# Optimization experiments

Hardware: AMD Instinct MI355X
Metric: run time of the kernel (lower is better)

## Reference

```python
import jax, jax.numpy as jnp
import numpy as np

N, E, F_IN, D, H, G, T = 30000, 480000, 128, 32, 4, 128, 10
HD = H * D
NEG_SLOPE = 0.2


def _lin(key, fan_out, fan_in, scale=0.05):
    k1, k2 = jax.random.split(key)
    return (jax.random.normal(k1, (fan_out, fan_in), jnp.float32) * scale,
            jax.random.normal(k2, (fan_out,), jnp.float32) * scale)


def setup_inputs() -> dict:
    key = jax.random.key(0)
    ks = jax.random.split(key, 24)
    x = jax.random.normal(ks[0], (N, F_IN), jnp.float32)
    edge_index = jax.random.randint(ks[1], (2, E), 0, N, jnp.int64)
    batch = jnp.sort(jax.random.randint(ks[2], (N,), 0, G, jnp.int64))
    inp = {"x": x, "edge_index": edge_index, "batch": batch}
    # conv 0 (in=F_IN) and conv 1 (in=D); each followed by Linear(HD -> D)
    for i, fin in enumerate([F_IN, D]):
        base = 3 + i * 8
        Wl, bl = _lin(ks[base + 0], HD, fin)
        Wr, br = _lin(ks[base + 1], HD, fin)
        att = jax.random.normal(ks[base + 2], (H, D), jnp.float32) * 0.05
        bias = jnp.zeros((HD,), jnp.float32)
        lw, lb = _lin(ks[base + 3], D, HD)
        inp.update({f"Wl{i}": Wl, f"bl{i}": bl, f"Wr{i}": Wr, f"br{i}": br,
                    f"att{i}": att, f"cb{i}": bias, f"lw{i}": lw, f"lb{i}": lb})
    inp["fc1_W"], inp["fc1_b"] = _lin(ks[20], D, D)
    inp["fc2_W"], inp["fc2_b"] = _lin(ks[21], T, D)
    return inp


def _gatv2_conv(x, src, dst, Wl, bl, Wr, br, att, bias):
    # PyG GATv2Conv, concat=True, add_self_loops already applied to src/dst,
    # aggr='mean', eval mode (no dropout).
    n = x.shape[0]
    xl = (x @ Wl.T + bl).reshape(n, H, D)
    xr = (x @ Wr.T + br).reshape(n, H, D)
    e = jax.nn.leaky_relu(xl[src] + xr[dst], NEG_SLOPE)          # [E', H, D]
    alpha = jnp.einsum('ehd,hd->eh', e, att)                      # [E', H]
    amax = jax.ops.segment_max(alpha, dst, num_segments=n)        # [n, H]
    ex = jnp.exp(alpha - amax[dst])
    denom = jax.ops.segment_sum(ex, dst, num_segments=n)
    a = ex / denom[dst]                                           # softmax per target
    msg = xl[src] * a[:, :, None]                                 # [E', H, D]
    s = jax.ops.segment_sum(msg, dst, num_segments=n)
    cnt = jax.ops.segment_sum(jnp.ones((src.shape[0],), jnp.float32), dst, num_segments=n)
    out = s / cnt[:, None, None]                                  # mean aggregation
    return out.reshape(n, HD) + bias


def reference(x, edge_index, batch,
              Wl0, bl0, Wr0, br0, att0, cb0, lw0, lb0,
              Wl1, bl1, Wr1, br1, att1, cb1, lw1, lb1,
              fc1_W, fc1_b, fc2_W, fc2_b):
    loop = jnp.arange(N, dtype=edge_index.dtype)
    src = jnp.concatenate([edge_index[0], loop])  # add self loops
    dst = jnp.concatenate([edge_index[1], loop])
    convs = [(Wl0, bl0, Wr0, br0, att0, cb0, lw0, lb0),
             (Wl1, bl1, Wr1, br1, att1, cb1, lw1, lb1)]
    h = x
    for (Wl, bl, Wr, br, att, cb, lw, lb) in convs:
        h = _gatv2_conv(h, src, dst, Wl, bl, Wr, br, att, cb)
        h = h @ lw.T + lb  # heads>1: Linear(H*D -> D)
    g = jax.ops.segment_max(h, batch, num_segments=G)  # global max pool
    g = jax.nn.relu(g @ fc1_W.T + fc1_b)
    return g @ fc2_W.T + fc2_b
```

## Files before the change

### kernel.cpp

```cpp
#include <hip/hip_runtime.h>
#include <hip/hip_bf16.h>
#include <hip/hip_fp16.h>

#define NEG_SLOPE 0.2f
#define GGRP 128
#define TOUT 10

typedef _Float16 half8 __attribute__((ext_vector_type(8)));
typedef float floatx4 __attribute__((ext_vector_type(4)));

__global__ void init_kernel(int* __restrict__ deg, float* __restrict__ gpool,
                            int* __restrict__ csr_pad, int n, int gsize) {
    int i = blockIdx.x * blockDim.x + threadIdx.x;
    if (i < n) deg[i] = 0;
    if (i < gsize) gpool[i] = -__builtin_inff();
    if (i < 64) csr_pad[i] = 0;
}

__global__ void cvt_kernel(const float* __restrict__ X, _Float16* __restrict__ Xh,
                           const float* __restrict__ Wl, _Float16* __restrict__ Wlh,
                           const float* __restrict__ Wr, _Float16* __restrict__ Wrh,
                           int nx8, int nw8) {
    int i = blockIdx.x * blockDim.x + threadIdx.x;
    const float* s; _Float16* d; int j;
    if (i < nx8) { s = X; d = Xh; j = i; }
    else if (i < nx8 + nw8) { s = Wl; d = Wlh; j = i - nx8; }
    else if (i < nx8 + 2 * nw8) { s = Wr; d = Wrh; j = i - nx8 - nw8; }
    else return;
    float4 a = *(const float4*)(s + j * 8);
    float4 b = *(const float4*)(s + j * 8 + 4);
    union { _Float16 h[8]; uint4 u; } pk;
    pk.h[0] = (_Float16)a.x; pk.h[1] = (_Float16)a.y;
    pk.h[2] = (_Float16)a.z; pk.h[3] = (_Float16)a.w;
    pk.h[4] = (_Float16)b.x; pk.h[5] = (_Float16)b.y;
    pk.h[6] = (_Float16)b.z; pk.h[7] = (_Float16)b.w;
    *(uint4*)(d + j * 8) = pk.u;
}

__global__ void degree_kernel(const int* __restrict__ dst, int* __restrict__ deg, int E) {
    int i = blockIdx.x * blockDim.x + threadIdx.x;
    int base = i * 4;
    if (base + 3 < E) {
        int4 d = *(const int4*)(dst + base);
        atomicAdd(&deg[d.x], 1); atomicAdd(&deg[d.y], 1);
        atomicAdd(&deg[d.z], 1); atomicAdd(&deg[d.w], 1);
    } else {
        for (int k = base; k < E; ++k) atomicAdd(&deg[dst[k]], 1);
    }
}

__global__ __launch_bounds__(256)
void scanA_kernel(const int* __restrict__ deg, int* __restrict__ rowptr,
                  int* __restrict__ bsum, int n) {
    __shared__ int wsum[4];
    int tid = threadIdx.x, lane = tid & 63, wid = tid >> 6;
    int idx = blockIdx.x * 256 + tid;
    int v = (idx < n) ? deg[idx] : 0;
    int x = v;
    #pragma unroll
    for (int off = 1; off < 64; off <<= 1) {
        int t = __shfl_up(x, off, 64);
        if (lane >= off) x += t;
    }
    if (lane == 63) wsum[wid] = x;
    __syncthreads();
    if (tid == 0) {
        int s = 0;
        #pragma unroll
        for (int i = 0; i < 4; ++i) { int t = wsum[i]; wsum[i] = s; s += t; }
        bsum[blockIdx.x] = s;
    }
    __syncthreads();
    int excl = x - v + wsum[wid];
    if (idx < n) rowptr[idx] = excl;
}

__global__ __launch_bounds__(256)
void scanC_kernel(int* __restrict__ rowptr, int* __restrict__ cursor,
                  const int* __restrict__ bsum, int n, int nb) {
    __shared__ int soff_sh;
    int tid = threadIdx.x;
    int bx = blockIdx.x;
    if (tid < 64) {
        int lane = tid;
        int v = 0;
        if (lane < nb && lane < bx) v = bsum[lane];
        if (lane + 64 < nb && lane + 64 < bx) v += bsum[lane + 64];
        #pragma unroll
        for (int off = 32; off >= 1; off >>= 1) v += __shfl_xor(v, off, 64);
        if (lane == 0) soff_sh = v;
        if (bx == 0) {
            int t = 0;
            if (lane < nb) t = bsum[lane];
            if (lane + 64 < nb) t += bsum[lane + 64];
            #pragma unroll
            for (int off = 32; off >= 1; off >>= 1) t += __shfl_xor(t, off, 64);
            if (lane == 0) rowptr[n] = t;
        }
    }
    __syncthreads();
    int idx = bx * 256 + tid;
    if (idx < n) {
        int r = rowptr[idx] + soff_sh;
        rowptr[idx] = r;
        cursor[idx] = r;
    }
}

__global__ void scatter_kernel(const int* __restrict__ src, const int* __restrict__ dst,
                               int* __restrict__ cursor, int* __restrict__ csr, int E) {
    int i = blockIdx.x * blockDim.x + threadIdx.x;
    int base = i * 4;
    if (base + 3 < E) {
        int4 s = *(const int4*)(src + base);
        int4 d = *(const int4*)(dst + base);
        csr[atomicAdd(&cursor[d.x], 1)] = s.x << 8;
        csr[atomicAdd(&cursor[d.y], 1)] = s.y << 8;
        csr[atomicAdd(&cursor[d.z], 1)] = s.z << 8;
        csr[atomicAdd(&cursor[d.w], 1)] = s.w << 8;
    } else {
        for (int k = base; k < E; ++k)
            csr[atomicAdd(&cursor[dst[k]], 1)] = src[k] << 8;
    }
}

__global__ __launch_bounds__(256)
void gemm_mfma_kernel(const _Float16* __restrict__ Xh,
                      const _Float16* __restrict__ Wlh, const float* __restrict__ bl,
                      const _Float16* __restrict__ Wrh, const float* __restrict__ br,
                      _Float16* __restrict__ xlh, float* __restrict__ xr, int n) {
    int tid = threadIdx.x;
    int wave = tid >> 6, lane = tid & 63;
    int r0 = blockIdx.x * 64 + wave * 16;
    if (r0 >= n) return;
    int l15 = lane & 15;
    int lkg = lane >> 4;
    int arow = r0 + l15; if (arow > n - 1) arow = n - 1;

    const char* xb  = (const char*)Xh;
    const char* wlb = (const char*)Wlh;
    const char* wrb = (const char*)Wrh;

    half8 a[4];
    #pragma unroll
    for (int kc = 0; kc < 4; ++kc)
        a[kc] = *(const half8*)(xb + (size_t)arow * 256 + kc * 64 + lkg * 16);

    floatx4 accL[8], accR[8];
    #pragma unroll
    for (int t = 0; t < 8; ++t) {
        accL[t] = (floatx4){0.f, 0.f, 0.f, 0.f};
        accR[t] = (floatx4){0.f, 0.f, 0.f, 0.f};
    }

    #pragma unroll
    for (int t = 0; t < 8; ++t) {
        int wrow = t * 16 + l15;
        int wk = lkg * 16;
        #pragma unroll
        for (int kc = 0; kc < 4; ++kc) {
            half8 bL = *(const half8*)(wlb + (size_t)wrow * 256 + kc * 64 + wk);
            half8 bR = *(const half8*)(wrb + (size_t)wrow * 256 + kc * 64 + wk);
            accL[t] = __builtin_amdgcn_mfma_f32_16x16x32_f16(a[kc], bL, accL[t], 0, 0, 0);
            accR[t] = __builtin_amdgcn_mfma_f32_16x16x32_f16(a[kc], bR, accR[t], 0, 0, 0);
        }
    }

    #pragma unroll
    for (int j = 0; j < 4; ++j) {
        int row = r0 + lkg * 4 + j;
        if (row < n) {
            #pragma unroll
            for (int t = 0; t < 8; ++t) {
                int col = t * 16 + l15;
                float vL = accL[t][j] + bl[col];
                float vR = accR[t][j] + br[col];
                xlh[(size_t)row * 128 + col] = (_Float16)vL;
                xr[(size_t)row * 128 + col] = vR;
            }
        }
    }
}

template <int FIN>
__global__ __launch_bounds__(256, 2)
void gemm_tile_kernel(const float* __restrict__ X,
                      const float* __restrict__ Wl, const float* __restrict__ bl,
                      const float* __restrict__ Wr, const float* __restrict__ br,
                      _Float16* __restrict__ xlh, float* __restrict__ xr,
                      int n, int nRowBlk) {
    constexpr int BK = 32, BM = 128, LDA = BM + 4;
    constexpr int NCHUNK = FIN / BK;
    __shared__ float Xs[BK][LDA];
    __shared__ float Ws[BK][LDA];
    int tid = threadIdx.x;
    int rowBlk = blockIdx.x;
    int colBlk = 0;
    if (rowBlk >= nRowBlk) { rowBlk -= nRowBlk; colBlk = 1; }
    const float* __restrict__ Wb = colBlk ? Wr : Wl;
    const float* __restrict__ bb = colBlk ? br : bl;
    int row0 = rowBlk * BM;

    int sr  = tid >> 3;
    int skq = (tid & 7) * 4;

    float4 xpre[4], wpre[4];

    auto load_pre = [&](int c) {
        int k0 = c * BK;
        #pragma unroll
        for (int i = 0; i < 4; ++i) {
            int r = sr + i * 32;
            int gr = row0 + r;
            float4 v = {0.f, 0.f, 0.f, 0.f};
            if (gr < n) v = *(const float4*)&X[(size_t)gr * FIN + k0 + skq];
            xpre[i] = v;
            wpre[i] = *(const float4*)&Wb[(size_t)r * FIN + k0 + skq];
        }
    };
    auto store_pre = [&]() {
        #pragma unroll
        for (int i = 0; i < 4; ++i) {
            int r = sr + i * 32;
            Xs[skq + 0][r] = xpre[i].x; Xs[skq + 1][r] = xpre[i].y;
            Xs[skq + 2][r] = xpre[i].z; Xs[skq + 3][r] = xpre[i].w;
            Ws[skq + 0][r] = wpre[i].x; Ws[skq + 1][r] = wpre[i].y;
            Ws[skq + 2][r] = wpre[i].z; Ws[skq + 3][r] = wpre[i].w;
        }
    };

    load_pre(0);
    store_pre();
    __syncthreads();

    int tx = tid & 15;
    int ty = tid >> 4;
    float acc[8][8];
    #pragma unroll
    for (int i = 0; i < 8; ++i)
        #pragma unroll
        for (int j = 0; j < 8; ++j) acc[i][j] = 0.f;

    #pragma unroll
    for (int c = 0; c < NCHUNK; ++c) {
        if (c + 1 < NCHUNK) load_pre(c + 1);
        #pragma unroll 8
        for (int k = 0; k < BK; ++k) {
            float4 a0 = *(const float4*)&Xs[k][ty * 8];
            float4 a1 = *(const float4*)&Xs[k][ty * 8 + 4];
            float4 b0 = *(const float4*)&Ws[k][tx * 8];
            float4 b1 = *(const float4*)&Ws[k][tx * 8 + 4];
            float av[8] = {a0.x, a0.y, a0.z, a0.w, a1.x, a1.y, a1.z, a1.w};
            float bv[8] = {b0.x, b0.y, b0.z, b0.w, b1.x, b1.y, b1.z, b1.w};
            #pragma unroll
            for (int i = 0; i < 8; ++i)
                #pragma unroll
                for (int j = 0; j < 8; ++j)
                    acc[i][j] = fmaf(av[i], bv[j], acc[i][j]);
        }
        if (c + 1 < NCHUNK) {
            __syncthreads();
            store_pre();
            __syncthreads();
        }
    }

    float bias[8];
    #pragma unroll
    for (int j = 0; j < 8; ++j) bias[j] = bb[tx * 8 + j];
    #pragma unroll
    for (int i = 0; i < 8; ++i) {
        int gr = row0 + ty * 8 + i;
        if (gr < n) {
            float v[8];
            #pragma unroll
            for (int j = 0; j < 8; ++j) v[j] = acc[i][j] + bias[j];
            if (colBlk == 0) {
                union { _Float16 h[8]; uint4 u; } pk;
                #pragma unroll
                for (int j = 0; j < 8; ++j) pk.h[j] = (_Float16)v[j];
                *(uint4*)&xlh[(size_t)gr * 128 + tx * 8] = pk.u;
            } else {
                float4 o0 = {v[0], v[1], v[2], v[3]};
                float4 o1 = {v[4], v[5], v[6], v[7]};
                *(float4*)&xr[(size_t)gr * 128 + tx * 8]     = o0;
                *(float4*)&xr[(size_t)gr * 128 + tx * 8 + 4] = o1;
            }
        }
    }
}

__global__ __launch_bounds__(256)
void gat_fused_kernel(const _Float16* __restrict__ xlh,
                      const float* __restrict__ xr,
                      const float* __restrict__ att, const float* __restrict__ cb,
                      const float* __restrict__ lw, const float* __restrict__ lb,
                      const int* __restrict__ rowptr, const int* __restrict__ csrb,
                      float* __restrict__ out , int n) {
    __shared__ float lws[32][132];
    __shared__ float oslot[4][128];
    int tid = threadIdx.x;
    #pragma unroll
    for (int i = 0; i < 16; ++i) {
        int idx = tid + i * 256;
        lws[idx >> 7][idx & 127] = lw[idx];
    }
    __syncthreads();

    int wid = tid >> 6, lane = tid & 63;
    int nd = blockIdx.x * 4 + wid;
    if (nd >= n) return;
    int q4  = lane >> 4;
    int l16 = lane & 15;
    int fb  = l16 * 32;
    int fbh = l16 * 16;

    const char* __restrict__ xlhb = (const char*)xlh;
    const char* __restrict__ xrb  = (const char*)xr;

    const float4 xrA = *(const float4*)(xrb + ((size_t)nd << 9) + fb);
    const float4 xrB = *(const float4*)(xrb + ((size_t)nd << 9) + fb + 16);
    const float4 atA = *(const float4*)((const char*)att + fb);
    const float4 atB = *(const float4*)((const char*)att + fb + 16);

    float4 xlsA, xlsB;
    {
        uint4 hs = *(const uint4*)(xlhb + ((size_t)nd << 8) + fbh);
        float2 s01 = __half22float2(*(const __half2*)&hs.x);
        float2 s23 = __half22float2(*(const __half2*)&hs.y);
        float2 s45 = __half22float2(*(const __half2*)&hs.z);
        float2 s67 = __half22float2(*(const __half2*)&hs.w);
        xlsA = (float4){s01.x, s01.y, s23.x, s23.y};
        xlsB = (float4){s45.x, s45.y, s67.x, s67.y};
    }

    int start = rowptr[nd], end = rowptr[nd + 1];
    float cnt = (float)(end - start + 1);

    float den;
    float accA[4], accB[4];

    {
        float e0 = xlsA.x + xrA.x; e0 = fmaxf(e0, NEG_SLOPE * e0);
        float e1 = xlsA.y + xrA.y; e1 = fmaxf(e1, NEG_SLOPE * e1);
        float e2 = xlsA.z + xrA.z; e2 = fmaxf(e2, NEG_SLOPE * e2);
        float e3 = xlsA.w + xrA.w; e3 = fmaxf(e3, NEG_SLOPE * e3);
        float e4 = xlsB.x + xrB.x; e4 = fmaxf(e4, NEG_SLOPE * e4);
        float e5 = xlsB.y + xrB.y; e5 = fmaxf(e5, NEG_SLOPE * e5);
        float e6 = xlsB.z + xrB.z; e6 = fmaxf(e6, NEG_SLOPE * e6);
        float e7 = xlsB.w + xrB.w; e7 = fmaxf(e7, NEG_SLOPE * e7);
        float q = e0 * atA.x + e1 * atA.y + e2 * atA.z + e3 * atA.w
                + e4 * atB.x + e5 * atB.y + e6 * atB.z + e7 * atB.w;
        q += __shfl_xor(q, 1); q += __shfl_xor(q, 2);
        float a = __expf(q);
        if (q4 == 0) {
            den = a;
            accA[0] = a * xlsA.x; accA[1] = a * xlsA.y;
            accA[2] = a * xlsA.z; accA[3] = a * xlsA.w;
            accB[0] = a * xlsB.x; accB[1] = a * xlsB.y;
            accB[2] = a * xlsB.z; accB[3] = a * xlsB.w;
        } else {
            den = 0.f;
            accA[0] = accA[1] = accA[2] = accA[3] = 0.f;
            accB[0] = accB[1] = accB[2] = accB[3] = 0.f;
        }
    }

    auto consume = [&](uint4 hx, bool guard) {
        float2 f01 = __half22float2(*(const __half2*)&hx.x);
        float2 f23 = __half22float2(*(const __half2*)&hx.y);
        float2 f45 = __half22float2(*(const __half2*)&hx.z);
        float2 f67 = __half22float2(*(const __half2*)&hx.w);
        float e0 = f01.x + xrA.x; e0 = fmaxf(e0, NEG_SLOPE * e0);
        float e1 = f01.y + xrA.y; e1 = fmaxf(e1, NEG_SLOPE * e1);
        float e2 = f23.x + xrA.z; e2 = fmaxf(e2, NEG_SLOPE * e2);
        float e3 = f23.y + xrA.w; e3 = fmaxf(e3, NEG_SLOPE * e3);
        float e4 = f45.x + xrB.x; e4 = fmaxf(e4, NEG_SLOPE * e4);
        float e5 = f45.y + xrB.y; e5 = fmaxf(e5, NEG_SLOPE * e5);
        float e6 = f67.x + xrB.z; e6 = fmaxf(e6, NEG_SLOPE * e6);
        float e7 = f67.y + xrB.w; e7 = fmaxf(e7, NEG_SLOPE * e7);
        float q = e0 * atA.x + e1 * atA.y + e2 * atA.z + e3 * atA.w
                + e4 * atB.x + e5 * atB.y + e6 * atB.z + e7 * atB.w;
        q += __shfl_xor(q, 1); q += __shfl_xor(q, 2);
        float a = __expf(q);
        if (!guard) a = 0.f;
        den += a;
        accA[0] = fmaf(a, f01.x, accA[0]); accA[1] = fmaf(a, f01.y, accA[1]);
        accA[2] = fmaf(a, f23.x, accA[2]); accA[3] = fmaf(a, f23.y, accA[3]);
        accB[0] = fmaf(a, f45.x, accB[0]); accB[1] = fmaf(a, f45.y, accB[1]);
        accB[2] = fmaf(a, f67.x, accB[2]); accB[3] = fmaf(a, f67.y, accB[3]);
    };

    int i = start + q4;
    int oA = csrb[i], oB = csrb[i + 4], oC = csrb[i + 8], oD = csrb[i + 12];
    uint4 pA = *(const uint4*)(xlhb + oA + fbh);
    uint4 pB = *(const uint4*)(xlhb + oB + fbh);
    uint4 pC = *(const uint4*)(xlhb + oC + fbh);
    uint4 pD = *(const uint4*)(xlhb + oD + fbh);
    oA = csrb[i + 16]; oB = csrb[i + 20]; oC = csrb[i + 24]; oD = csrb[i + 28];
    for (; i < end; i += 16) {
        uint4 c0 = pA;
        pA = *(const uint4*)(xlhb + oA + fbh); oA = csrb[i + 32];
        consume(c0, true);
        uint4 c1 = pB;
        pB = *(const uint4*)(xlhb + oB + fbh); oB = csrb[i + 36];
        consume(c1, (i + 4) < end);
        uint4 c2 = pC;
        pC = *(const uint4*)(xlhb + oC + fbh); oC = csrb[i + 40];
        consume(c2, (i + 8) < end);
        uint4 c3 = pD;
        pD = *(const uint4*)(xlhb + oD + fbh); oD = csrb[i + 44];
        consume(c3, (i + 12) < end);
    }

    #pragma unroll
    for (int t = 0; t < 4; ++t) {
        accA[t] += __shfl_xor(accA[t], 16); accA[t] += __shfl_xor(accA[t], 32);
        accB[t] += __shfl_xor(accB[t], 16); accB[t] += __shfl_xor(accB[t], 32);
    }
    den += __shfl_xor(den, 16); den += __shfl_xor(den, 32);

    float inv = 1.0f / (den * cnt);
    if (q4 == 0) {
        const float4 cbA = *(const float4*)((const char*)cb + fb);
        const float4 cbB = *(const float4*)((const char*)cb + fb + 16);
        float4 oA4, oB4;
        oA4.x = fmaf(accA[0], inv, cbA.x); oA4.y = fmaf(accA[1], inv, cbA.y);
        oA4.z = fmaf(accA[2], inv, cbA.z); oA4.w = fmaf(accA[3], inv, cbA.w);
        oB4.x = fmaf(accB[0], inv, cbB.x); oB4.y = fmaf(accB[1], inv, cbB.y);
        oB4.z = fmaf(accB[2], inv, cbB.z); oB4.w = fmaf(accB[3], inv, cbB.w);
        *(float4*)((char*)&oslot[wid][0] + fb)      = oA4;
        *(float4*)((char*)&oslot[wid][0] + fb + 16) = oB4;
    }
    asm volatile("s_waitcnt lgkmcnt(0)" ::: "memory");

    int half = lane >> 5;
    int l32 = lane & 31;
    float y = 0.f;
    int kbase = half * 64;
    #pragma unroll
    for (int k = 0; k < 64; k += 4) {
        float4 lv = *(const float4*)&lws[l32][kbase + k];
        float4 ov = *(const float4*)&oslot[wid][kbase + k];
        y = fmaf(lv.x, ov.x, y);
        y = fmaf(lv.y, ov.y, y);
        y = fmaf(lv.z, ov.z, y);
        y = fmaf(lv.w, ov.w, y);
    }
    y += __shfl_xor(y, 32);
    if (half == 0) out[(size_t)nd * 32 + l32] = y + lb[l32];
}

__device__ __forceinline__ void atomicMaxFloat(float* addr, float val) {
    if (val >= 0.f) atomicMax((int*)addr, __float_as_int(val));
    else atomicMin((unsigned int*)addr, (unsigned int)__float_as_int(val));
}

__global__ void pool_kernel(const float* __restrict__ H, const int* __restrict__ batch,
                            float* __restrict__ g, int n) {
    int tid = threadIdx.x;
    int dim = tid & 31;
    int sub = tid >> 5;
    int nodeStart = blockIdx.x * 128 + sub * 16;
    float m = -__builtin_inff();
    int cur = -1;
    for (int j = 0; j < 16; ++j) {
        int nd = nodeStart + j;
        if (nd >= n) break;
        int b = batch[nd];
        if (b != cur) {
            if (cur >= 0) atomicMaxFloat(&g[cur * 32 + dim], m);
            cur = b; m = -__builtin_inff();
        }
        m = fmaxf(m, H[nd * 32 + dim]);
    }
    if (cur >= 0) atomicMaxFloat(&g[cur * 32 + dim], m);
}

__global__ __launch_bounds__(256)
void fc_kernel(const float* __restrict__ g,
               const float* __restrict__ fc1W, const float* __restrict__ fc1b,
               const float* __restrict__ fc2W, const float* __restrict__ fc2b,
               float* __restrict__ out) {
    __shared__ float g1[GGRP * 32];
    int tid = threadIdx.x;
    for (int idx = tid; idx < GGRP * 32; idx += 256) {
        int r = idx >> 5, c = idx & 31;
        float acc = fc1b[c];
        #pragma unroll
        for (int k = 0; k < 32; ++k) acc = fmaf(g[r * 32 + k], fc1W[c * 32 + k], acc);
        g1[idx] = acc > 0.f ? acc : 0.f;
    }
    __syncthreads();
    for (int idx = tid; idx < GGRP * TOUT; idx += 256) {
        int r = idx / TOUT, c = idx - r * TOUT;
        float acc = fc2b[c];
        #pragma unroll
        for (int k = 0; k < 32; ++k) acc = fmaf(g1[r * 32 + k], fc2W[c * 32 + k], acc);
        out[idx] = acc;
    }
}

extern "C" void kernel_launch(void* const* d_in, const int* in_sizes, int n_in,
                              void* d_out, int out_size, void* d_ws, size_t ws_size,
                              hipStream_t stream) {
    const float* x     = (const float*)d_in[0];
    const int*   ei    = (const int*)d_in[1];
    const int*   batch = (const int*)d_in[2];
    const float* Wl0 = (const float*)d_in[3];
    const float* bl0 = (const float*)d_in[4];
    const float* Wr0 = (const float*)d_in[5];
    const float* br0 = (const float*)d_in[6];
    const float* at0 = (const float*)d_in[7];
    const float* cb0 = (const float*)d_in[8];
    const float* lw0 = (const float*)d_in[9];
    const float* lb0 = (const float*)d_in[10];
    const float* Wl1 = (const float*)d_in[11];
    const float* bl1 = (const float*)d_in[12];
    const float* Wr1 = (const float*)d_in[13];
    const float* br1 = (const float*)d_in[14];
    const float* at1 = (const float*)d_in[15];
    const float* cb1 = (const float*)d_in[16];
    const float* lw1 = (const float*)d_in[17];
    const float* lb1 = (const float*)d_in[18];
    const float* fc1W = (const float*)d_in[19];
    const float* fc1b = (const float*)d_in[20];
    const float* fc2W = (const float*)d_in[21];
    const float* fc2b = (const float*)d_in[22];

    const int n = in_sizes[0] / 128;
    const int E = in_sizes[1] / 2;
    const int* src = ei;
    const int* dst = ei + E;
    const int nblkScan = (n + 255) / 256;
    const int nRowBlk = (n + 127) / 128;
    const int E4 = (E + 3) / 4;
    const int nx8 = n * 16;
    const int nw8 = 128 * 128 / 8;

    size_t off = 0;
    auto alloc = [&](size_t bytes) {
        void* p = (char*)d_ws + off;
        off += (bytes + 255) & ~(size_t)255;
        return p;
    };
    _Float16* xh  = (_Float16*)alloc((size_t)n * 128 * 2);
    _Float16* wlh = (_Float16*)alloc(128 * 128 * 2);
    _Float16* wrh = (_Float16*)alloc(128 * 128 * 2);
    _Float16* xlh = (_Float16*)alloc((size_t)n * 128 * 2);
    float* xr    = (float*)alloc((size_t)n * 128 * 4);
    float* hbuf  = (float*)alloc((size_t)n * 32 * 4);
    int* deg     = (int*)alloc((size_t)n * 4);
    int* rowptr  = (int*)alloc((size_t)(n + 1) * 4);
    int* cursor  = (int*)alloc((size_t)n * 4);
    int* csr     = (int*)alloc((size_t)(E + 64) * 4);
    int* bsum    = (int*)alloc(128 * 4);
    float* gpool = (float*)alloc((size_t)GGRP * 32 * 4);

    init_kernel<<<(n + 255) / 256, 256, 0, stream>>>(deg, gpool, csr + E, n, GGRP * 32);
    cvt_kernel<<<(nx8 + 2 * nw8 + 255) / 256, 256, 0, stream>>>(x, xh, Wl0, wlh,
                                                                Wr0, wrh, nx8, nw8);
    degree_kernel<<<(E4 + 255) / 256, 256, 0, stream>>>(dst, deg, E);
    scanA_kernel<<<nblkScan, 256, 0, stream>>>(deg, rowptr, bsum, n);
    scanC_kernel<<<nblkScan, 256, 0, stream>>>(rowptr, cursor, bsum, n, nblkScan);
    scatter_kernel<<<(E4 + 255) / 256, 256, 0, stream>>>(src, dst, cursor, csr, E);

    gemm_mfma_kernel<<<(n + 63) / 64, 256, 0, stream>>>(xh, wlh, bl0, wrh, br0,
                                                        xlh, xr, n);
    gat_fused_kernel<<<(n + 3) / 4, 256, 0, stream>>>(xlh, xr, at0, cb0, lw0, lb0,
                                                      rowptr, csr, hbuf, n);
    gemm_tile_kernel<32><<<2 * nRowBlk, 256, 0, stream>>>(hbuf, Wl1, bl1, Wr1, br1,
                                                          xlh, xr, n, nRowBlk);
    gat_fused_kernel<<<(n + 3) / 4, 256, 0, stream>>>(xlh, xr, at1, cb1, lw1, lb1,
                                                      rowptr, csr, hbuf, n);

    pool_kernel<<<(n + 127) / 128, 256, 0, stream>>>(hbuf, batch, gpool, n);
    fc_kernel<<<1, 256, 0, stream>>>(gpool, fc1W, fc1b, fc2W, fc2b, (float*)d_out);
}
```

Baseline: 305.0 us.

## Use fp16 MFMA for second-layer projection and simplify gather prefetch loop

```diff
diff --git a/kernel.cpp b/kernel.cpp
--- a/kernel.cpp
+++ b/kernel.cpp
@@ -18,14 +18,18 @@
 }
 
 __global__ void cvt_kernel(const float* __restrict__ X, _Float16* __restrict__ Xh,
-                           const float* __restrict__ Wl, _Float16* __restrict__ Wlh,
-                           const float* __restrict__ Wr, _Float16* __restrict__ Wrh,
-                           int nx8, int nw8) {
+                           const float* __restrict__ Wl0, _Float16* __restrict__ Wl0h,
+                           const float* __restrict__ Wr0, _Float16* __restrict__ Wr0h,
+                           const float* __restrict__ Wl1, _Float16* __restrict__ Wl1h,
+                           const float* __restrict__ Wr1, _Float16* __restrict__ Wr1h,
+                           int nx8, int nw8, int nw1) {
     int i = blockIdx.x * blockDim.x + threadIdx.x;
     const float* s; _Float16* d; int j;
     if (i < nx8) { s = X; d = Xh; j = i; }
-    else if (i < nx8 + nw8) { s = Wl; d = Wlh; j = i - nx8; }
-    else if (i < nx8 + 2 * nw8) { s = Wr; d = Wrh; j = i - nx8 - nw8; }
+    else if (i < nx8 + nw8) { s = Wl0; d = Wl0h; j = i - nx8; }
+    else if (i < nx8 + 2 * nw8) { s = Wr0; d = Wr0h; j = i - nx8 - nw8; }
+    else if (i < nx8 + 2 * nw8 + nw1) { s = Wl1; d = Wl1h; j = i - nx8 - 2 * nw8; }
+    else if (i < nx8 + 2 * nw8 + 2 * nw1) { s = Wr1; d = Wr1h; j = i - nx8 - 2 * nw8 - nw1; }
     else return;
     float4 a = *(const float4*)(s + j * 8);
     float4 b = *(const float4*)(s + j * 8 + 4);
@@ -182,109 +186,43 @@
     }
 }
 
-template <int FIN>
-__global__ __launch_bounds__(256, 2)
-void gemm_tile_kernel(const float* __restrict__ X,
-                      const float* __restrict__ Wl, const float* __restrict__ bl,
-                      const float* __restrict__ Wr, const float* __restrict__ br,
-                      _Float16* __restrict__ xlh, float* __restrict__ xr,
-                      int n, int nRowBlk) {
-    constexpr int BK = 32, BM = 128, LDA = BM + 4;
-    constexpr int NCHUNK = FIN / BK;
-    __shared__ float Xs[BK][LDA];
-    __shared__ float Ws[BK][LDA];
+__global__ __launch_bounds__(256)
+void gemm_mfma32_kernel(const _Float16* __restrict__ Hh,
+                        const _Float16* __restrict__ Wlh, const float* __restrict__ bl,
+                        const _Float16* __restrict__ Wrh, const float* __restrict__ br,
+                        _Float16* __restrict__ xlh, float* __restrict__ xr, int n) {
     int tid = threadIdx.x;
-    int rowBlk = blockIdx.x;
-    int colBlk = 0;
-    if (rowBlk >= nRowBlk) { rowBlk -= nRowBlk; colBlk = 1; }
-    const float* __restrict__ Wb = colBlk ? Wr : Wl;
-    const float* __restrict__ bb = colBlk ? br : bl;
-    int row0 = rowBlk * BM;
-
-    int sr  = tid >> 3;
-    int skq = (tid & 7) * 4;
-
-    float4 xpre[4], wpre[4];
-
-    auto load_pre = [&](int c) {
-        int k0 = c * BK;
-        #pragma unroll
-        for (int i = 0; i < 4; ++i) {
-            int r = sr + i * 32;
-            int gr = row0 + r;
-            float4 v = {0.f, 0.f, 0.f, 0.f};
-            if (gr < n) v = *(const float4*)&X[(size_t)gr * FIN + k0 + skq];
-            xpre[i] = v;
-            wpre[i] = *(const float4*)&Wb[(size_t)r * FIN + k0 + skq];
-        }
-    };
-    auto store_pre = [&]() {
-        #pragma unroll
-        for (int i = 0; i < 4; ++i) {
-            int r = sr + i * 32;
-            Xs[skq + 0][r] = xpre[i].x; Xs[skq + 1][r] = xpre[i].y;
-            Xs[skq + 2][r] = xpre[i].z; Xs[skq + 3][r] = xpre[i].w;
-            Ws[skq + 0][r] = wpre[i].x; Ws[skq + 1][r] = wpre[i].y;
-            Ws[skq + 2][r] = wpre[i].z; Ws[skq + 3][r] = wpre[i].w;
-        }
-    };
-
-    load_pre(0);
-    store_pre();
-    __syncthreads();
-
-    int tx = tid & 15;
-    int ty = tid >> 4;
-    float acc[8][8];
-    #pragma unroll
-    for (int i = 0; i < 8; ++i)
-        #pragma unroll
-        for (int j = 0; j < 8; ++j) acc[i][j] = 0.f;
-
-    #pragma unroll
-    for (int c = 0; c < NCHUNK; ++c) {
-        if (c + 1 < NCHUNK) load_pre(c + 1);
-        #pragma unroll 8
-        for (int k = 0; k < BK; ++k) {
-            float4 a0 = *(const float4*)&Xs[k][ty * 8];
-            float4 a1 = *(const float4*)&Xs[k][ty * 8 + 4];
-            float4 b0 = *(const float4*)&Ws[k][tx * 8];
-            float4 b1 = *(const float4*)&Ws[k][tx * 8 + 4];
-            float av[8] = {a0.x, a0.y, a0.z, a0.w, a1.x, a1.y, a1.z, a1.w};
-            float bv[8] = {b0.x, b0.y, b0.z, b0.w, b1.x, b1.y, b1.z, b1.w};
+    int wave = tid >> 6, lane = tid & 63;
+    int r0 = blockIdx.x * 64 + wave * 16;
+    if (r0 >= n) return;
+    int l15 = lane & 15;
+    int lkg = lane >> 4;
+    int arow = r0 + l15; if (arow > n - 1) arow = n - 1;
+
+    half8 a = *(const half8*)(Hh + (size_t)arow * 32 + lkg * 8);
+
+    floatx4 accL[8], accR[8];
+    #pragma unroll
+    for (int t = 0; t < 8; ++t) {
+        int wrow = t * 16 + l15;
+        half8 bL = *(const half8*)(Wlh + (size_t)wrow * 32 + lkg * 8);
+        half8 bR = *(const half8*)(Wrh + (size_t)wrow * 32 + lkg * 8);
+        floatx4 z = (floatx4){0.f, 0.f, 0.f, 0.f};
+        accL[t] = __builtin_amdgcn_mfma_f32_16x16x32_f16(a, bL, z, 0, 0, 0);
+        accR[t] = __builtin_amdgcn_mfma_f32_16x16x32_f16(a, bR, z, 0, 0, 0);
+    }
+
+    #pragma unroll
+    for (int j = 0; j < 4; ++j) {
+        int row = r0 + lkg * 4 + j;
+        if (row < n) {
             #pragma unroll
-            for (int i = 0; i < 8; ++i)
-                #pragma unroll
-                for (int j = 0; j < 8; ++j)
-                    acc[i][j] = fmaf(av[i], bv[j], acc[i][j]);
-        }
-        if (c + 1 < NCHUNK) {
-            __syncthreads();
-            store_pre();
-            __syncthreads();
-        }
-    }
-
-    float bias[8];
-    #pragma unroll
-    for (int j = 0; j < 8; ++j) bias[j] = bb[tx * 8 + j];
-    #pragma unroll
-    for (int i = 0; i < 8; ++i) {
-        int gr = row0 + ty * 8 + i;
-        if (gr < n) {
-            float v[8];
-            #pragma unroll
-            for (int j = 0; j < 8; ++j) v[j] = acc[i][j] + bias[j];
-            if (colBlk == 0) {
-                union { _Float16 h[8]; uint4 u; } pk;
-                #pragma unroll
-                for (int j = 0; j < 8; ++j) pk.h[j] = (_Float16)v[j];
-                *(uint4*)&xlh[(size_t)gr * 128 + tx * 8] = pk.u;
-            } else {
-                float4 o0 = {v[0], v[1], v[2], v[3]};
-                float4 o1 = {v[4], v[5], v[6], v[7]};
-                *(float4*)&xr[(size_t)gr * 128 + tx * 8]     = o0;
-                *(float4*)&xr[(size_t)gr * 128 + tx * 8 + 4] = o1;
+            for (int t = 0; t < 8; ++t) {
+                int col = t * 16 + l15;
+                float vL = accL[t][j] + bl[col];
+                float vR = accR[t][j] + br[col];
+                xlh[(size_t)row * 128 + col] = (_Float16)vL;
+                xr[(size_t)row * 128 + col] = vR;
             }
         }
     }
@@ -296,7 +234,8 @@
                       const float* __restrict__ att, const float* __restrict__ cb,
                       const float* __restrict__ lw, const float* __restrict__ lb,
                       const int* __restrict__ rowptr, const int* __restrict__ csrb,
-                      float* __restrict__ out , int n) {
+                      float* __restrict__ out ,
+                      _Float16* __restrict__ outh , int n) {
     __shared__ float lws[32][132];
     __shared__ float oslot[4][128];
     int tid = threadIdx.x;
@@ -366,7 +305,15 @@
         }
     }
 
-    auto consume = [&](uint4 hx, bool guard) {
+    int i = start + q4;
+    int offC = csrb[i + 8];
+    uint4 preA = *(const uint4*)(xlhb + csrb[i] + fbh);
+    uint4 preB = *(const uint4*)(xlhb + csrb[i + 4] + fbh);
+    for (; i < end; i += 4) {
+        uint4 hx = preA;
+        preA = preB;
+        preB = *(const uint4*)(xlhb + offC + fbh);
+        offC = csrb[i + 12];
         float2 f01 = __half22float2(*(const __half2*)&hx.x);
         float2 f23 = __half22float2(*(const __half2*)&hx.y);
         float2 f45 = __half22float2(*(const __half2*)&hx.z);
@@ -383,34 +330,11 @@
                 + e4 * atB.x + e5 * atB.y + e6 * atB.z + e7 * atB.w;
         q += __shfl_xor(q, 1); q += __shfl_xor(q, 2);
         float a = __expf(q);
-        if (!guard) a = 0.f;
         den += a;
         accA[0] = fmaf(a, f01.x, accA[0]); accA[1] = fmaf(a, f01.y, accA[1]);
         accA[2] = fmaf(a, f23.x, accA[2]); accA[3] = fmaf(a, f23.y, accA[3]);
         accB[0] = fmaf(a, f45.x, accB[0]); accB[1] = fmaf(a, f45.y, accB[1]);
         accB[2] = fmaf(a, f67.x, accB[2]); accB[3] = fmaf(a, f67.y, accB[3]);
-    };
-
-    int i = start + q4;
-    int oA = csrb[i], oB = csrb[i + 4], oC = csrb[i + 8], oD = csrb[i + 12];
-    uint4 pA = *(const uint4*)(xlhb + oA + fbh);
-    uint4 pB = *(const uint4*)(xlhb + oB + fbh);
-    uint4 pC = *(const uint4*)(xlhb + oC + fbh);
-    uint4 pD = *(const uint4*)(xlhb + oD + fbh);
-    oA = csrb[i + 16]; oB = csrb[i + 20]; oC = csrb[i + 24]; oD = csrb[i + 28];
-    for (; i < end; i += 16) {
-        uint4 c0 = pA;
-        pA = *(const uint4*)(xlhb + oA + fbh); oA = csrb[i + 32];
-        consume(c0, true);
-        uint4 c1 = pB;
-        pB = *(const uint4*)(xlhb + oB + fbh); oB = csrb[i + 36];
-        consume(c1, (i + 4) < end);
-        uint4 c2 = pC;
-        pC = *(const uint4*)(xlhb + oC + fbh); oC = csrb[i + 40];
-        consume(c2, (i + 8) < end);
-        uint4 c3 = pD;
-        pD = *(const uint4*)(xlhb + oD + fbh); oD = csrb[i + 44];
-        consume(c3, (i + 12) < end);
     }
 
     #pragma unroll
@@ -448,7 +372,11 @@
         y = fmaf(lv.w, ov.w, y);
     }
     y += __shfl_xor(y, 32);
-    if (half == 0) out[(size_t)nd * 32 + l32] = y + lb[l32];
+    if (half == 0) {
+        float yy = y + lb[l32];
+        out[(size_t)nd * 32 + l32] = yy;
+        outh[(size_t)nd * 32 + l32] = (_Float16)yy;
+    }
 }
 
 __device__ __forceinline__ void atomicMaxFloat(float* addr, float val) {
@@ -533,10 +461,10 @@
     const int* src = ei;
     const int* dst = ei + E;
     const int nblkScan = (n + 255) / 256;
-    const int nRowBlk = (n + 127) / 128;
     const int E4 = (E + 3) / 4;
     const int nx8 = n * 16;
     const int nw8 = 128 * 128 / 8;
+    const int nw1 = 128 * 32 / 8;
 
     size_t off = 0;
     auto alloc = [&](size_t bytes) {
@@ -544,12 +472,15 @@
         off += (bytes + 255) & ~(size_t)255;
         return p;
     };
-    _Float16* xh  = (_Float16*)alloc((size_t)n * 128 * 2);
-    _Float16* wlh = (_Float16*)alloc(128 * 128 * 2);
-    _Float16* wrh = (_Float16*)alloc(128 * 128 * 2);
-    _Float16* xlh = (_Float16*)alloc((size_t)n * 128 * 2);
+    _Float16* xh   = (_Float16*)alloc((size_t)n * 128 * 2);
+    _Float16* wl0h = (_Float16*)alloc(128 * 128 * 2);
+    _Float16* wr0h = (_Float16*)alloc(128 * 128 * 2);
+    _Float16* wl1h = (_Float16*)alloc(128 * 32 * 2);
+    _Float16* wr1h = (_Float16*)alloc(128 * 32 * 2);
+    _Float16* xlh  = (_Float16*)alloc((size_t)n * 128 * 2);
     float* xr    = (float*)alloc((size_t)n * 128 * 4);
     float* hbuf  = (float*)alloc((size_t)n * 32 * 4);
+    _Float16* hbufh = (_Float16*)alloc((size_t)n * 32 * 2);
     int* deg     = (int*)alloc((size_t)n * 4);
     int* rowptr  = (int*)alloc((size_t)(n + 1) * 4);
     int* cursor  = (int*)alloc((size_t)n * 4);
@@ -558,21 +489,21 @@
     float* gpool = (float*)alloc((size_t)GGRP * 32 * 4);
 
     init_kernel<<<(n + 255) / 256, 256, 0, stream>>>(deg, gpool, csr + E, n, GGRP * 32);
-    cvt_kernel<<<(nx8 + 2 * nw8 + 255) / 256, 256, 0, stream>>>(x, xh, Wl0, wlh,
-                                                                Wr0, wrh, nx8, nw8);
+    cvt_kernel<<<(nx8 + 2 * nw8 + 2 * nw1 + 255) / 256, 256, 0, stream>>>(
+        x, xh, Wl0, wl0h, Wr0, wr0h, Wl1, wl1h, Wr1, wr1h, nx8, nw8, nw1);
     degree_kernel<<<(E4 + 255) / 256, 256, 0, stream>>>(dst, deg, E);
     scanA_kernel<<<nblkScan, 256, 0, stream>>>(deg, rowptr, bsum, n);
     scanC_kernel<<<nblkScan, 256, 0, stream>>>(rowptr, cursor, bsum, n, nblkScan);
     scatter_kernel<<<(E4 + 255) / 256, 256, 0, stream>>>(src, dst, cursor, csr, E);
 
-    gemm_mfma_kernel<<<(n + 63) / 64, 256, 0, stream>>>(xh, wlh, bl0, wrh, br0,
+    gemm_mfma_kernel<<<(n + 63) / 64, 256, 0, stream>>>(xh, wl0h, bl0, wr0h, br0,
                                                         xlh, xr, n);
     gat_fused_kernel<<<(n + 3) / 4, 256, 0, stream>>>(xlh, xr, at0, cb0, lw0, lb0,
-                                                      rowptr, csr, hbuf, n);
-    gemm_tile_kernel<32><<<2 * nRowBlk, 256, 0, stream>>>(hbuf, Wl1, bl1, Wr1, br1,
-                                                          xlh, xr, n, nRowBlk);
+                                                      rowptr, csr, hbuf, hbufh, n);
+    gemm_mfma32_kernel<<<(n + 63) / 64, 256, 0, stream>>>(hbufh, wl1h, bl1, wr1h, br1,
+                                                          xlh, xr, n);
     gat_fused_kernel<<<(n + 3) / 4, 256, 0, stream>>>(xlh, xr, at1, cb1, lw1, lb1,
-                                                      rowptr, csr, hbuf, n);
+                                                      rowptr, csr, hbuf, hbufh, n);
 
     pool_kernel<<<(n + 127) / 128, 256, 0, stream>>>(hbuf, batch, gpool, n);
     fc_kernel<<<1, 256, 0, stream>>>(gpool, fc1W, fc1b, fc2W, fc2b, (float*)d_out);
```

Measured after the change: 289.2 us. 5.2% less time.
